# Optimization experiments

Measured on AMD Instinct MI355X. Metric: run time of the kernel, lower is better.

## Reference

```python
import jax, jax.numpy as jnp
import numpy as np

N_NODES = 50000
N_EDGES = 800000
IN_NODE = 256
IN_EDGE = 64
OUT_DIM = 128


def setup_inputs() -> dict:
    key = jax.random.key(0)
    k1, k2, k3, k4, k5, k6, k7 = jax.random.split(key, 7)
    feats_node = jax.random.normal(k1, (N_NODES, IN_NODE), dtype=jnp.float32)
    feats_edge = jax.random.normal(k2, (N_EDGES, IN_EDGE), dtype=jnp.float32)
    src = jax.random.randint(k3, (N_EDGES,), 0, N_NODES, dtype=jnp.int32)
    dst = jax.random.randint(k4, (N_EDGES,), 0, N_NODES, dtype=jnp.int32)
    # weights init: normal(std=0.5), torch Linear stores [out, in]
    Wn = 0.5 * jax.random.normal(k5, (OUT_DIM, IN_NODE), dtype=jnp.float32)
    We = 0.5 * jax.random.normal(k6, (IN_EDGE, IN_EDGE), dtype=jnp.float32)
    Wa = 0.5 * jax.random.normal(k7, (1, 2 * OUT_DIM + IN_EDGE), dtype=jnp.float32)
    return {"feats_node": feats_node, "feats_edge": feats_edge,
            "src": src, "dst": dst, "Wn": Wn, "We": We, "Wa": Wa}


def reference(feats_node, feats_edge, src, dst, Wn, We, Wa):
    n_nodes = feats_node.shape[0]
    # node / edge projections
    z = feats_node @ Wn.T            # [N, out_dim]
    ze = feats_edge @ We.T           # [E, in_dim_edge]
    # per-edge attention logit: attn_fc(cat(z_src, z_dst, z_edge)) + leaky_relu
    z3 = jnp.concatenate([z[src], z[dst], ze], axis=1)   # [E, 2*out+edge]
    a = z3 @ Wa.T                                        # [E, 1]
    e = jax.nn.leaky_relu(a, negative_slope=0.2)[:, 0]   # [E]
    # segment softmax over incoming edges of each dst node (numerically stable)
    m = jax.ops.segment_max(e, dst, num_segments=n_nodes)        # [N]
    m = jnp.where(jnp.isfinite(m), m, 0.0)                       # isolated nodes
    e_exp = jnp.exp(e - m[dst])                                  # [E]
    denom = jax.ops.segment_sum(e_exp, dst, num_segments=n_nodes)  # [N]
    alpha = e_exp / jnp.maximum(denom[dst], 1e-38)               # [E]
    # weighted scatter-sum of source messages
    h = jax.ops.segment_sum(alpha[:, None] * z[src], dst, num_segments=n_nodes)
    return h, ze
```

## Files before the change

kernel.cpp:

```cpp
#include <hip/hip_runtime.h>
#include <hip/hip_bf16.h>
#include <math.h>

#define N_NODES 50000
#define N_EDGES 800000
#define IN_NODE 256
#define IN_EDGE 64
#define OUT_DIM 128

typedef __attribute__((ext_vector_type(8))) short short8;
typedef __attribute__((ext_vector_type(4))) float f32x4;

__device__ inline short f2bf(float x) {
    union { float f; unsigned u; } v; v.f = x;
    unsigned r = v.u + 0x7fff + ((v.u >> 16) & 1);
    return (short)(r >> 16);
}

__device__ inline void cvt_store8(short* p, float4 a, float4 b) {
    union { short h[8]; uint4 u; } t;
    t.h[0] = f2bf(a.x); t.h[1] = f2bf(a.y); t.h[2] = f2bf(a.z); t.h[3] = f2bf(a.w);
    t.h[4] = f2bf(b.x); t.h[5] = f2bf(b.y); t.h[6] = f2bf(b.z); t.h[7] = f2bf(b.w);
    *(uint4*)p = t.u;
}

__global__ void k0_ve(const float* __restrict__ We, const float* __restrict__ Wa,
                      float* __restrict__ v_e)
{
    const int k = threadIdx.x;
    if (k < IN_EDGE) {
        float s = 0.f;
        for (int c = 0; c < IN_EDGE; ++c)
            s += We[c * IN_EDGE + k] * Wa[2 * OUT_DIM + c];
        v_e[k] = s;
    }
}

#define K1_MT 64
#define K1_KT 32

__global__ __launch_bounds__(256) void k1_node_gemm(
    const float* __restrict__ fn, const float* __restrict__ Wn,
    const float* __restrict__ Wa,
    __hip_bfloat16* __restrict__ zb,
    float* __restrict__ s_src, float* __restrict__ s_dst)
{
    __shared__ float A_s[K1_KT][K1_MT + 4];
    __shared__ float B_s[K1_KT][OUT_DIM + 4];
    __shared__ float red_s[K1_MT][17];
    __shared__ float red_d[K1_MT][17];

    const int t  = threadIdx.x;
    const int m0 = blockIdx.x * K1_MT;
    const int tn = t & 15;
    const int tm = t >> 4;
    const int r0 = tm * 4;
    const int c0 = tn * 8;

    float acc[4][8];
    for (int i = 0; i < 4; ++i)
        for (int j = 0; j < 8; ++j) acc[i][j] = 0.f;

    for (int k0 = 0; k0 < IN_NODE; k0 += K1_KT) {
        {
            const int chunk = t & 7;
            const int nd    = t >> 3;
            for (int hh = 0; hh < 2; ++hh) {
                const int node = nd + hh * 32;
                int gr = m0 + node; if (gr >= N_NODES) gr = N_NODES - 1;
                const float4 v = *(const float4*)&fn[(size_t)gr * IN_NODE + k0 + chunk * 4];
                A_s[chunk * 4 + 0][node] = v.x;
                A_s[chunk * 4 + 1][node] = v.y;
                A_s[chunk * 4 + 2][node] = v.z;
                A_s[chunk * 4 + 3][node] = v.w;
            }
        }
        {
            const int chunk = t & 7;
            const int cb    = t >> 3;
            for (int hh = 0; hh < 4; ++hh) {
                const int c = cb + hh * 32;
                const float4 v = *(const float4*)&Wn[(size_t)c * IN_NODE + k0 + chunk * 4];
                B_s[chunk * 4 + 0][c] = v.x;
                B_s[chunk * 4 + 1][c] = v.y;
                B_s[chunk * 4 + 2][c] = v.z;
                B_s[chunk * 4 + 3][c] = v.w;
            }
        }
        __syncthreads();

        for (int k = 0; k < K1_KT; ++k) {
            const float4 a  = *(const float4*)&A_s[k][r0];
            const float4 b0 = *(const float4*)&B_s[k][c0];
            const float4 b1 = *(const float4*)&B_s[k][c0 + 4];
            const float av[4] = {a.x, a.y, a.z, a.w};
            const float bv[8] = {b0.x, b0.y, b0.z, b0.w, b1.x, b1.y, b1.z, b1.w};
            for (int i = 0; i < 4; ++i)
                for (int j = 0; j < 8; ++j)
                    acc[i][j] += av[i] * bv[j];
        }
        __syncthreads();
    }

    float wa_s[8], wa_d[8];
    for (int j = 0; j < 8; ++j) {
        wa_s[j] = Wa[c0 + j];
        wa_d[j] = Wa[OUT_DIM + c0 + j];
    }
    float ps[4], pd[4];
    for (int i = 0; i < 4; ++i) {
        float a = 0.f, b = 0.f;
        for (int j = 0; j < 8; ++j) {
            a += wa_s[j] * acc[i][j];
            b += wa_d[j] * acc[i][j];
        }
        ps[i] = a; pd[i] = b;
    }

    for (int i = 0; i < 4; ++i) {
        const int node = m0 + r0 + i;
        if (node < N_NODES) {
            alignas(16) __hip_bfloat16 tmp[8];
            for (int j = 0; j < 8; ++j) tmp[j] = __float2bfloat16(acc[i][j]);
            *(uint4*)&zb[(size_t)node * OUT_DIM + c0] = *(const uint4*)tmp;
        }
    }

    for (int i = 0; i < 4; ++i) {
        red_s[r0 + i][tn] = ps[i];
        red_d[r0 + i][tn] = pd[i];
    }
    __syncthreads();
    if (t < K1_MT) {
        const int node = m0 + t;
        if (node < N_NODES) {
            float a = 0.f, b = 0.f;
            for (int j = 0; j < 16; ++j) { a += red_s[t][j]; b += red_d[t][j]; }
            s_src[node] = a;
            s_dst[node] = b;
        }
    }
}

__global__ __launch_bounds__(256) void k2_edge_gemm_mfma(
    const float* __restrict__ fe, const float* __restrict__ We,
    const float* __restrict__ v_e,
    const int* __restrict__ dst, int* __restrict__ deg,
    float* __restrict__ ze_out, float* __restrict__ s_e)
{
    __shared__ alignas(16) short A_lds[128][72];
    __shared__ alignas(16) short B_lds[64][72];

    const int t    = threadIdx.x;
    const int lane = t & 63;
    const int w    = t >> 6;
    const long e0  = (long)blockIdx.x * 128;

    if (t < 128) atomicAdd(&deg[dst[e0 + t]], 1);

    {
        const int edge = t >> 1, half = t & 1;
        const float4* rp = (const float4*)&fe[(e0 + edge) * IN_EDGE + half * 32];
        float4 va[8];
        for (int q = 0; q < 8; ++q) va[q] = rp[q];

        float part = 0.f;
        for (int q = 0; q < 8; ++q) {
            const float4 w4 = *(const float4*)&v_e[half * 32 + q * 4];
            part += va[q].x * w4.x + va[q].y * w4.y
                  + va[q].z * w4.z + va[q].w * w4.w;
        }
        const float other = __shfl_xor(part, 1, 64);
        if (half == 0) s_e[e0 + edge] = part + other;

        short* wp = &A_lds[edge][half * 32];
        for (int q = 0; q < 4; ++q)
            cvt_store8(wp + q * 8, va[2 * q], va[2 * q + 1]);
    }
    {
        const int row = t >> 2, kq = (t & 3) * 16;
        const float4* rp = (const float4*)&We[(size_t)row * IN_EDGE + kq];
        cvt_store8(&B_lds[row][kq + 0], rp[0], rp[1]);
        cvt_store8(&B_lds[row][kq + 8], rp[2], rp[3]);
    }
    __syncthreads();

    const int lrow = lane & 15;
    const int lk   = (lane >> 4) * 8;

    f32x4 acc[2][4];
    for (int r = 0; r < 2; ++r)
        for (int c = 0; c < 4; ++c)
            acc[r][c] = (f32x4){0.f, 0.f, 0.f, 0.f};

    for (int s = 0; s < 2; ++s) {
        const int kk = s * 32 + lk;
        short8 aF[2], bF[4];
        for (int r = 0; r < 2; ++r)
            aF[r] = *(const short8*)&A_lds[w * 32 + r * 16 + lrow][kk];
        for (int c = 0; c < 4; ++c)
            bF[c] = *(const short8*)&B_lds[c * 16 + lrow][kk];
        for (int r = 0; r < 2; ++r)
            for (int c = 0; c < 4; ++c)
                acc[r][c] = __builtin_amdgcn_mfma_f32_16x16x32_bf16(
                    aF[r], bF[c], acc[r][c], 0, 0, 0);
    }

    const int rquad = lane >> 4;
    for (int r = 0; r < 2; ++r) {
        for (int c = 0; c < 4; ++c) {
            for (int reg = 0; reg < 4; ++reg) {
                const long row = e0 + w * 32 + r * 16 + rquad * 4 + reg;
                ze_out[row * IN_EDGE + c * 16 + lrow] = acc[r][c][reg];
            }
        }
    }
}

#define SCAN_T 1024
#define SCAN_C 49

__global__ __launch_bounds__(SCAN_T) void k4_scan(
    const int* __restrict__ deg, int* __restrict__ off, int* __restrict__ cursor)
{
    __shared__ int part[SCAN_T];
    const int t = threadIdx.x;
    const int lo = t * SCAN_C;
    int hi = lo + SCAN_C; if (hi > N_NODES) hi = N_NODES;

    int s = 0;
    for (int i = lo; i < hi; ++i) s += deg[i];
    part[t] = s;
    __syncthreads();
    for (int d = 1; d < SCAN_T; d <<= 1) {
        int v = 0;
        if (t >= d) v = part[t - d];
        __syncthreads();
        if (t >= d) part[t] += v;
        __syncthreads();
    }
    int run = (t == 0) ? 0 : part[t - 1];
    for (int i = lo; i < hi; ++i) {
        off[i] = run; cursor[i] = run;
        run += deg[i];
    }
    if (t == SCAN_T - 1) off[N_NODES] = part[SCAN_T - 1];
}

__global__ void k5_fill(
    const int* __restrict__ src, const int* __restrict__ dst,
    const float* __restrict__ s_src, const float* __restrict__ s_dst,
    const float* __restrict__ s_e, int* __restrict__ cursor,
    int* __restrict__ csr_src, float* __restrict__ csr_e)
{
    const int i = blockIdx.x * blockDim.x + threadIdx.x;
    if (i >= N_EDGES) return;
    const int d = dst[i];
    const int s = src[i];
    const int pos = atomicAdd(&cursor[d], 1);
    csr_src[pos] = s;
    float e = s_src[s] + s_dst[d] + s_e[i];
    e = (e > 0.f) ? e : 0.2f * e;
    csr_e[pos] = e;
}

__global__ __launch_bounds__(256) void k6_aggregate(
    const int* __restrict__ off, const int* __restrict__ csr_src,
    const float* __restrict__ csr_e, const __hip_bfloat16* __restrict__ zb,
    float* __restrict__ h)
{
    const int wave = (int)((blockIdx.x * blockDim.x + threadIdx.x) >> 6);
    const int lane = threadIdx.x & 63;
    if (wave >= N_NODES) return;

    const int beg = off[wave];
    const int end = off[wave + 1];
    const int deg = end - beg;

    float2 acc = make_float2(0.f, 0.f);
    if (deg > 0) {
        float m = -INFINITY;
        for (int j = lane; j < deg; j += 64) m = fmaxf(m, csr_e[beg + j]);
        for (int o = 32; o > 0; o >>= 1) m = fmaxf(m, __shfl_xor(m, o, 64));

        float l = 0.f;
        for (int j = 0; j < deg; ++j) {
            const int s = csr_src[beg + j];
            const float w = __expf(csr_e[beg + j] - m);
            l += w;
            const __hip_bfloat162 zp =
                *(const __hip_bfloat162*)&zb[(size_t)s * OUT_DIM + lane * 2];
            const float2 zv = __bfloat1622float2(zp);
            acc.x += w * zv.x;
            acc.y += w * zv.y;
        }
        const float inv = 1.f / fmaxf(l, 1e-38f);
        acc.x *= inv; acc.y *= inv;
    }
    *(float2*)&h[(size_t)wave * OUT_DIM + lane * 2] = acc;
}

extern "C" void kernel_launch(void* const* d_in, const int* in_sizes, int n_in,
                              void* d_out, int out_size, void* d_ws, size_t ws_size,
                              hipStream_t stream)
{
    const float* fn  = (const float*)d_in[0];
    const float* fe  = (const float*)d_in[1];
    const int*   src = (const int*)d_in[2];
    const int*   dst = (const int*)d_in[3];
    const float* Wn  = (const float*)d_in[4];
    const float* We  = (const float*)d_in[5];
    const float* Wa  = (const float*)d_in[6];

    float* h_out  = (float*)d_out;
    float* ze_out = h_out + (size_t)N_NODES * OUT_DIM;

    char* p = (char*)d_ws;
    auto alloc = [&](size_t bytes) -> char* {
        char* r = p;
        p += (bytes + 255) & ~(size_t)255;
        return r;
    };
    __hip_bfloat16* zb = (__hip_bfloat16*)alloc((size_t)N_NODES * OUT_DIM * 2);
    float* s_src   = (float*)alloc((size_t)N_NODES * 4);
    float* s_dst   = (float*)alloc((size_t)N_NODES * 4);
    float* s_e     = (float*)alloc((size_t)N_EDGES * 4);
    int*   deg     = (int*)alloc((size_t)N_NODES * 4);
    int*   off     = (int*)alloc((size_t)(N_NODES + 1) * 4);
    int*   cursor  = (int*)alloc((size_t)N_NODES * 4);
    int*   csr_src = (int*)alloc((size_t)N_EDGES * 4);
    float* csr_e   = (float*)alloc((size_t)N_EDGES * 4);
    float* v_e     = (float*)alloc((size_t)IN_EDGE * 4);

    hipMemsetAsync(deg, 0, (size_t)N_NODES * sizeof(int), stream);

    k0_ve<<<1, 64, 0, stream>>>(We, Wa, v_e);
    k1_node_gemm<<<(N_NODES + K1_MT - 1) / K1_MT, 256, 0, stream>>>(
        fn, Wn, Wa, zb, s_src, s_dst);
    k2_edge_gemm_mfma<<<N_EDGES / 128, 256, 0, stream>>>(
        fe, We, v_e, dst, deg, ze_out, s_e);
    k4_scan<<<1, SCAN_T, 0, stream>>>(deg, off, cursor);
    k5_fill<<<(N_EDGES + 255) / 256, 256, 0, stream>>>(
        src, dst, s_src, s_dst, s_e, cursor, csr_src, csr_e);
    k6_aggregate<<<(N_NODES + 3) / 4, 256, 0, stream>>>(
        off, csr_src, csr_e, zb, h_out);
}
```

Before: 712.1 us.

## Fuse CSR fill into edge GEMM and vectorize per-node aggregation

Degree counting moves into a separate vectorized kernel that runs before the edge GEMM, so the scan finishes before k2. k2 can then compute each edge's logit and do the CSR scatter itself, which removes the k5_fill kernel and the s_e round trip through global memory. The aggregation kernel now has each wave process 4 edges at a time, with 16 lanes each loading 16-byte bf16 chunks. Weights are computed once per 64-edge chunk and broadcast by shuffle, followed by a cross-lane reduction. The risks are an extra kernel launch and atomics inside the GEMM kernel.

```diff
diff --git a/kernel.cpp b/kernel.cpp
--- a/kernel.cpp
+++ b/kernel.cpp
@@ -33,6 +33,19 @@
         for (int c = 0; c < IN_EDGE; ++c)
             s += We[c * IN_EDGE + k] * Wa[2 * OUT_DIM + c];
         v_e[k] = s;
+    }
+}
+
+__global__ __launch_bounds__(256) void k_deg(const int* __restrict__ dst,
+                                             int* __restrict__ deg)
+{
+    const int i = (blockIdx.x * 256 + threadIdx.x) * 4;
+    if (i < N_EDGES) {
+        const int4 d = *(const int4*)&dst[i];
+        atomicAdd(&deg[d.x], 1);
+        atomicAdd(&deg[d.y], 1);
+        atomicAdd(&deg[d.z], 1);
+        atomicAdd(&deg[d.w], 1);
     }
 }
 
@@ -145,18 +158,20 @@
 __global__ __launch_bounds__(256) void k2_edge_gemm_mfma(
     const float* __restrict__ fe, const float* __restrict__ We,
     const float* __restrict__ v_e,
-    const int* __restrict__ dst, int* __restrict__ deg,
-    float* __restrict__ ze_out, float* __restrict__ s_e)
+    const int* __restrict__ src, const int* __restrict__ dst,
+    const float* __restrict__ s_src, const float* __restrict__ s_dst,
+    int* __restrict__ cursor,
+    float* __restrict__ ze_out, int* __restrict__ csr_src,
+    float* __restrict__ csr_e)
 {
     __shared__ alignas(16) short A_lds[128][72];
     __shared__ alignas(16) short B_lds[64][72];
+    __shared__ float se_lds[128];
 
     const int t    = threadIdx.x;
     const int lane = t & 63;
     const int w    = t >> 6;
     const long e0  = (long)blockIdx.x * 128;
-
-    if (t < 128) atomicAdd(&deg[dst[e0 + t]], 1);
 
     {
         const int edge = t >> 1, half = t & 1;
@@ -171,7 +186,7 @@
                   + va[q].z * w4.z + va[q].w * w4.w;
         }
         const float other = __shfl_xor(part, 1, 64);
-        if (half == 0) s_e[e0 + edge] = part + other;
+        if (half == 0) se_lds[edge] = part + other;
 
         short* wp = &A_lds[edge][half * 32];
         for (int q = 0; q < 4; ++q)
@@ -215,6 +230,17 @@
             }
         }
     }
+
+    if (t < 128) {
+        const long e = e0 + t;
+        const int d = dst[e];
+        const int s = src[e];
+        float lg = s_src[s] + s_dst[d] + se_lds[t];
+        lg = (lg > 0.f) ? lg : 0.2f * lg;
+        const int pos = atomicAdd(&cursor[d], 1);
+        csr_src[pos] = s;
+        csr_e[pos]   = lg;
+    }
 }
 
 #define SCAN_T 1024
@@ -247,57 +273,68 @@
     if (t == SCAN_T - 1) off[N_NODES] = part[SCAN_T - 1];
 }
 
-__global__ void k5_fill(
-    const int* __restrict__ src, const int* __restrict__ dst,
-    const float* __restrict__ s_src, const float* __restrict__ s_dst,
-    const float* __restrict__ s_e, int* __restrict__ cursor,
-    int* __restrict__ csr_src, float* __restrict__ csr_e)
-{
-    const int i = blockIdx.x * blockDim.x + threadIdx.x;
-    if (i >= N_EDGES) return;
-    const int d = dst[i];
-    const int s = src[i];
-    const int pos = atomicAdd(&cursor[d], 1);
-    csr_src[pos] = s;
-    float e = s_src[s] + s_dst[d] + s_e[i];
-    e = (e > 0.f) ? e : 0.2f * e;
-    csr_e[pos] = e;
-}
-
 __global__ __launch_bounds__(256) void k6_aggregate(
     const int* __restrict__ off, const int* __restrict__ csr_src,
     const float* __restrict__ csr_e, const __hip_bfloat16* __restrict__ zb,
     float* __restrict__ h)
 {
-    const int wave = (int)((blockIdx.x * blockDim.x + threadIdx.x) >> 6);
+    const int node = (int)((blockIdx.x * blockDim.x + threadIdx.x) >> 6);
     const int lane = threadIdx.x & 63;
-    if (wave >= N_NODES) return;
-
-    const int beg = off[wave];
-    const int end = off[wave + 1];
+    if (node >= N_NODES) return;
+
+    const int beg = off[node];
+    const int end = off[node + 1];
     const int deg = end - beg;
 
-    float2 acc = make_float2(0.f, 0.f);
+    const int cgrp = lane & 15;
+    const int eidx = lane >> 4;
+
+    float out[8] = {0.f, 0.f, 0.f, 0.f, 0.f, 0.f, 0.f, 0.f};
+
     if (deg > 0) {
         float m = -INFINITY;
         for (int j = lane; j < deg; j += 64) m = fmaxf(m, csr_e[beg + j]);
         for (int o = 32; o > 0; o >>= 1) m = fmaxf(m, __shfl_xor(m, o, 64));
 
         float l = 0.f;
-        for (int j = 0; j < deg; ++j) {
-            const int s = csr_src[beg + j];
-            const float w = __expf(csr_e[beg + j] - m);
-            l += w;
-            const __hip_bfloat162 zp =
-                *(const __hip_bfloat162*)&zb[(size_t)s * OUT_DIM + lane * 2];
-            const float2 zv = __bfloat1622float2(zp);
-            acc.x += w * zv.x;
-            acc.y += w * zv.y;
+        for (int c0 = 0; c0 < deg; c0 += 64) {
+            const int cl = min(64, deg - c0);
+            float wv = 0.f;
+            if (lane < cl) wv = __expf(csr_e[beg + c0 + lane] - m);
+            float ws = wv;
+            for (int o = 32; o > 0; o >>= 1) ws += __shfl_xor(ws, o, 64);
+            l += ws;
+
+            for (int jj = 0; jj < cl; jj += 4) {
+                const int j  = jj + eidx;
+                const int jc = (j < cl) ? j : (cl - 1);
+                const float wgt = __shfl(wv, jc, 64);
+                if (j < cl) {
+                    const int s = csr_src[beg + c0 + j];
+                    const uint4 zv = *(const uint4*)&zb[(size_t)s * OUT_DIM + cgrp * 8];
+                    const unsigned* zu = (const unsigned*)&zv;
+                    for (int q = 0; q < 4; ++q) {
+                        out[2 * q]     += wgt * __uint_as_float(zu[q] << 16);
+                        out[2 * q + 1] += wgt * __uint_as_float(zu[q] & 0xffff0000u);
+                    }
+                }
+            }
+        }
+        for (int i = 0; i < 8; ++i) {
+            out[i] += __shfl_xor(out[i], 16, 64);
+            out[i] += __shfl_xor(out[i], 32, 64);
         }
         const float inv = 1.f / fmaxf(l, 1e-38f);
-        acc.x *= inv; acc.y *= inv;
-    }
-    *(float2*)&h[(size_t)wave * OUT_DIM + lane * 2] = acc;
+        for (int i = 0; i < 8; ++i) out[i] *= inv;
+    }
+
+    if (lane < 16) {
+        float4 o0 = make_float4(out[0], out[1], out[2], out[3]);
+        float4 o1 = make_float4(out[4], out[5], out[6], out[7]);
+        float* hp = &h[(size_t)node * OUT_DIM + lane * 8];
+        *(float4*)(hp + 0) = o0;
+        *(float4*)(hp + 4) = o1;
+    }
 }
 
 extern "C" void kernel_launch(void* const* d_in, const int* in_sizes, int n_in,
@@ -324,7 +361,6 @@
     __hip_bfloat16* zb = (__hip_bfloat16*)alloc((size_t)N_NODES * OUT_DIM * 2);
     float* s_src   = (float*)alloc((size_t)N_NODES * 4);
     float* s_dst   = (float*)alloc((size_t)N_NODES * 4);
-    float* s_e     = (float*)alloc((size_t)N_EDGES * 4);
     int*   deg     = (int*)alloc((size_t)N_NODES * 4);
     int*   off     = (int*)alloc((size_t)(N_NODES + 1) * 4);
     int*   cursor  = (int*)alloc((size_t)N_NODES * 4);
@@ -335,13 +371,12 @@
     hipMemsetAsync(deg, 0, (size_t)N_NODES * sizeof(int), stream);
 
     k0_ve<<<1, 64, 0, stream>>>(We, Wa, v_e);
+    k_deg<<<(N_EDGES / 4 + 255) / 256, 256, 0, stream>>>(dst, deg);
+    k4_scan<<<1, SCAN_T, 0, stream>>>(deg, off, cursor);
     k1_node_gemm<<<(N_NODES + K1_MT - 1) / K1_MT, 256, 0, stream>>>(
         fn, Wn, Wa, zb, s_src, s_dst);
     k2_edge_gemm_mfma<<<N_EDGES / 128, 256, 0, stream>>>(
-        fe, We, v_e, dst, deg, ze_out, s_e);
-    k4_scan<<<1, SCAN_T, 0, stream>>>(deg, off, cursor);
-    k5_fill<<<(N_EDGES + 255) / 256, 256, 0, stream>>>(
-        src, dst, s_src, s_dst, s_e, cursor, csr_src, csr_e);
+        fe, We, v_e, src, dst, s_src, s_dst, cursor, ze_out, csr_src, csr_e);
     k6_aggregate<<<(N_NODES + 3) / 4, 256, 0, stream>>>(
         off, csr_src, csr_e, zb, h_out);
 }
```

Result: faster. 686.6 us (-3.6%).
